# Optimization experiments

Measured on AMD Instinct MI355X. Metric: run time of the kernel, lower is better.

## Reference

```python
import jax, jax.numpy as jnp
import numpy as np

ALPHA_MARGIN = 1.0


def setup_inputs() -> dict:
    key = jax.random.key(0)
    k1, k2 = jax.random.split(key)
    B, N, H = 32, 128, 128  # batch, num_node, num_hidden
    X = jax.random.normal(k1, (B, N * N, 2 * H), dtype=jnp.float32)
    y = jax.random.randint(k2, (B, N, N), 0, 2, dtype=jnp.int32)
    return {"X": X, "y": y}


def reference(X, y):
    B, P, D = X.shape
    H = D // 2
    # split pair embeddings: e_a = X[..., :H], e_b = X[..., H:]
    diff = X[:, :, :H] - X[:, :, H:]
    dist2 = jnp.sum(diff * diff, axis=-1)  # (B, N*N) squared L2 distance
    adj = y.reshape(B, P)  # pair i corresponds to (i // N, i % N) == row-major flatten
    pos_loss = dist2
    neg_loss = jnp.maximum(ALPHA_MARGIN - dist2, 0.0)
    # entries untouched by the original loop (adj not in {0,1}) remain 0
    loss = jnp.where(adj == 1, pos_loss, jnp.where(adj == 0, neg_loss, 0.0))
    return loss
```

## Files before the change

### kernel.cpp

```cpp
#include <hip/hip_runtime.h>
#include <hip/hip_bf16.h>

#define ALPHA_MARGIN 1.0f

__global__ __launch_bounds__(256) void closs_kernel(
        const float4* __restrict__ X4,
        const int*    __restrict__ y,
        float*        __restrict__ out,
        int n_pairs) {
    int wave = (int)((blockIdx.x * blockDim.x + threadIdx.x) >> 6);
    int lane = threadIdx.x & 63;
    if (wave >= n_pairs) return;

    float4 v = X4[(size_t)wave * 64 + lane];

    float ox = __shfl_xor(v.x, 32);
    float oy = __shfl_xor(v.y, 32);
    float oz = __shfl_xor(v.z, 32);
    float ow = __shfl_xor(v.w, 32);

    float dx = v.x - ox;
    float dy = v.y - oy;
    float dz = v.z - oz;
    float dw = v.w - ow;
    float s = dx * dx + dy * dy + dz * dz + dw * dw;

    #pragma unroll
    for (int m = 16; m >= 1; m >>= 1)
        s += __shfl_xor(s, m);

    if (lane == 0) {
        int adj = y[wave];
        float loss;
        if (adj == 1)      loss = s;
        else if (adj == 0) loss = fmaxf(ALPHA_MARGIN - s, 0.0f);
        else               loss = 0.0f;
        out[wave] = loss;
    }
}

extern "C" void kernel_launch(void* const* d_in, const int* in_sizes, int n_in,
                              void* d_out, int out_size, void* d_ws, size_t ws_size,
                              hipStream_t stream) {
    const float* X = (const float*)d_in[0];
    const int*   y = (const int*)d_in[1];
    float* out = (float*)d_out;

    int n_pairs = in_sizes[1];
    int blocks = (n_pairs + 3) / 4;

    closs_kernel<<<blocks, 256, 0, stream>>>((const float4*)X, y, out, n_pairs);
}
```

Baseline: 670.0 us.

## Use persistent grid-stride waves with batched nontemporal loads of four pairs

```diff
diff --git a/kernel.cpp b/kernel.cpp
--- a/kernel.cpp
+++ b/kernel.cpp
@@ -3,39 +3,46 @@
 
 #define ALPHA_MARGIN 1.0f
 
+typedef float f32x4 __attribute__((ext_vector_type(4)));
+
 __global__ __launch_bounds__(256) void closs_kernel(
-        const float4* __restrict__ X4,
-        const int*    __restrict__ y,
-        float*        __restrict__ out,
+        const f32x4* __restrict__ X4,
+        const int*   __restrict__ y,
+        float*       __restrict__ out,
         int n_pairs) {
-    int wave = (int)((blockIdx.x * blockDim.x + threadIdx.x) >> 6);
-    int lane = threadIdx.x & 63;
-    if (wave >= n_pairs) return;
+    const int tid    = blockIdx.x * blockDim.x + threadIdx.x;
+    const int wave   = tid >> 6;
+    const int lane   = threadIdx.x & 63;
+    const int nwaves = (gridDim.x * blockDim.x) >> 6;
+    const int stride = nwaves * 4;
 
-    float4 v = X4[(size_t)wave * 64 + lane];
-
-    float ox = __shfl_xor(v.x, 32);
-    float oy = __shfl_xor(v.y, 32);
-    float oz = __shfl_xor(v.z, 32);
-    float ow = __shfl_xor(v.w, 32);
-
-    float dx = v.x - ox;
-    float dy = v.y - oy;
-    float dz = v.z - oz;
-    float dw = v.w - ow;
-    float s = dx * dx + dy * dy + dz * dz + dw * dw;
-
-    #pragma unroll
-    for (int m = 16; m >= 1; m >>= 1)
-        s += __shfl_xor(s, m);
-
-    if (lane == 0) {
-        int adj = y[wave];
-        float loss;
-        if (adj == 1)      loss = s;
-        else if (adj == 0) loss = fmaxf(ALPHA_MARGIN - s, 0.0f);
-        else               loss = 0.0f;
-        out[wave] = loss;
+    for (int base = wave; base < n_pairs; base += stride) {
+        f32x4 v[4];
+        #pragma unroll
+        for (int k = 0; k < 4; ++k) {
+            int p = base + k * nwaves;
+            if (p < n_pairs)
+                v[k] = __builtin_nontemporal_load(&X4[(size_t)p * 64 + lane]);
+        }
+        #pragma unroll
+        for (int k = 0; k < 4; ++k) {
+            int p = base + k * nwaves;
+            if (p >= n_pairs) break;
+            float dx = v[k][0] - __shfl_xor(v[k][0], 32);
+            float dy = v[k][1] - __shfl_xor(v[k][1], 32);
+            float dz = v[k][2] - __shfl_xor(v[k][2], 32);
+            float dw = v[k][3] - __shfl_xor(v[k][3], 32);
+            float s = dx * dx + dy * dy + dz * dz + dw * dw;
+            #pragma unroll
+            for (int m = 16; m >= 1; m >>= 1)
+                s += __shfl_xor(s, m);
+            if (lane == 0) {
+                int adj = y[p];
+                float loss = (adj == 1) ? s
+                           : (adj == 0 ? fmaxf(ALPHA_MARGIN - s, 0.0f) : 0.0f);
+                __builtin_nontemporal_store(loss, &out[p]);
+            }
+        }
     }
 }
 
@@ -47,7 +54,7 @@
     float* out = (float*)d_out;
 
     int n_pairs = in_sizes[1];
-    int blocks = (n_pairs + 3) / 4;
 
-    closs_kernel<<<blocks, 256, 0, stream>>>((const float4*)X, y, out, n_pairs);
+    int blocks = 2048;
+    closs_kernel<<<blocks, 256, 0, stream>>>((const f32x4*)X, y, out, n_pairs);
 }
```

After: 682.4 us. No clear change (+1.9%).
